# Optimization experiments

Hardware: AMD Instinct MI355X
Metric: run time of the kernel (lower is better)

## Reference

```python
import jax, jax.numpy as jnp
import numpy as np

LABELS_NUM_COUNT = [500000, 120000, 80000, 45000, 30000, 250000, 15000, 9000,
                    60000, 7000, 180000, 22000, 11000, 95000, 5000, 40000]
B, W = 2097152, 16  # batch, num_classes


def _build_penalty_matrix():
    c = np.asarray(LABELS_NUM_COUNT, dtype=np.float32)
    P = np.maximum(c[:, None], c[None, :]) / (c[:, None] + c[None, :])
    np.fill_diagonal(P, 1.0)
    return jnp.asarray(P)  # [W, W]


def setup_inputs() -> dict:
    key = jax.random.key(0)
    k1, k2 = jax.random.split(key)
    predict = jax.random.normal(k1, (B, W), dtype=jnp.float32)
    target = jax.random.normal(k2, (B, W), dtype=jnp.float32)
    return {"predict": predict, "target": target,
            "penalty_matrix": _build_penalty_matrix()}


def reference(predict, target, penalty_matrix):
    # `logpredict` in the original is actually softmax(predict).
    probs = jax.nn.softmax(predict, axis=-1)              # [B, W]
    pre = jnp.argmax(predict, axis=-1)                    # [B] predicted class
    tar = jnp.argmax(target, axis=-1)                     # [B] target class
    # scatter_ writes 1 at the predicted slot, then the loop overwrites it with
    # penalty[tar, pre] on mismatch or 0 on match -> net weight is:
    w = jnp.where(pre == tar, jnp.float32(0.0), penalty_matrix[tar, pre])  # [B]
    # sum(onehot * probs, -1) == probs at the predicted class
    p_at_pre = jnp.take_along_axis(probs, pre[:, None], axis=-1)[:, 0]     # [B]
    return jnp.mean(w * p_at_pre)
```

## Files before the change

kernel.cpp:

```cpp
#include <hip/hip_runtime.h>

#define NROWS 2097152
#define W 16

__global__ __launch_bounds__(256) void cel_weight_kernel(
    const float* __restrict__ predict,
    const float* __restrict__ target,
    const float* __restrict__ penalty,
    float* __restrict__ out)
{
    __shared__ float s_pen[W * W];
    __shared__ float s_part[4];

    const int tid = threadIdx.x;
    if (tid < W * W) s_pen[tid] = penalty[tid];
    __syncthreads();

    float acc = 0.0f;
    const int stride = gridDim.x * blockDim.x;

    for (int r = blockIdx.x * blockDim.x + tid; r < NROWS; r += stride) {
        const float4* prow = (const float4*)(predict + (size_t)r * W);
        const float4* trow = (const float4*)(target + (size_t)r * W);
        float4 p0 = prow[0], p1 = prow[1], p2 = prow[2], p3 = prow[3];
        float4 t0 = trow[0], t1 = trow[1], t2 = trow[2], t3 = trow[3];

        float pv[W] = {p0.x, p0.y, p0.z, p0.w, p1.x, p1.y, p1.z, p1.w,
                       p2.x, p2.y, p2.z, p2.w, p3.x, p3.y, p3.z, p3.w};
        float tv[W] = {t0.x, t0.y, t0.z, t0.w, t1.x, t1.y, t1.z, t1.w,
                       t2.x, t2.y, t2.z, t2.w, t3.x, t3.y, t3.z, t3.w};

        float pmax = pv[0]; int pidx = 0;
        #pragma unroll
        for (int j = 1; j < W; ++j) {
            if (pv[j] > pmax) { pmax = pv[j]; pidx = j; }
        }
        float s = 0.0f;
        #pragma unroll
        for (int j = 0; j < W; ++j) s += __expf(pv[j] - pmax);

        float tmax = tv[0]; int tidx = 0;
        #pragma unroll
        for (int j = 1; j < W; ++j) {
            if (tv[j] > tmax) { tmax = tv[j]; tidx = j; }
        }

        float wgt = (pidx == tidx) ? 0.0f : s_pen[tidx * W + pidx];
        acc += wgt / s;
    }

    #pragma unroll
    for (int off = 32; off > 0; off >>= 1)
        acc += __shfl_down(acc, off);

    const int lane = tid & 63;
    const int wid  = tid >> 6;
    if (lane == 0) s_part[wid] = acc;
    __syncthreads();

    if (tid == 0) {
        float tot = s_part[0] + s_part[1] + s_part[2] + s_part[3];
        atomicAdd(out, tot * (1.0f / (float)NROWS));
    }
}

extern "C" void kernel_launch(void* const* d_in, const int* in_sizes, int n_in,
                              void* d_out, int out_size, void* d_ws, size_t ws_size,
                              hipStream_t stream)
{
    const float* predict = (const float*)d_in[0];
    const float* target  = (const float*)d_in[1];
    const float* penalty = (const float*)d_in[2];
    float* out = (float*)d_out;

    hipMemsetAsync(out, 0, sizeof(float) * out_size, stream);

    dim3 grid(2048), block(256);
    cel_weight_kernel<<<grid, block, 0, stream>>>(predict, target, penalty, out);
}
```

Baseline: 274.4 us.

## Split each row across four lanes with shuffle-based argmax and softmax reductions

Reassigns work so four consecutive lanes each load one float4 of a row, which makes global loads fully coalesced instead of each thread reading a 64-byte row. Per-row max, argmax and exp-sum are combined across the four lanes with xor shuffles, and four independent loads are issued per iteration to raise memory-level parallelism. The cost is extra shuffle instructions, with three of every four lanes sitting idle during accumulation. The iteration count is fixed at compile time.

```diff
diff --git a/kernel.cpp b/kernel.cpp
--- a/kernel.cpp
+++ b/kernel.cpp
@@ -2,54 +2,81 @@
 
 #define NROWS 2097152
 #define W 16
+#define TPB 256
+#define BLOCKS 2048
+#define STRIDE (BLOCKS * TPB)
+#define NF4 (NROWS * 4)
+#define NITER (NF4 / STRIDE)
+#define UNROLL 4
 
-__global__ __launch_bounds__(256) void cel_weight_kernel(
+__device__ __forceinline__ void argmax_combine(float& m, int& i, float mo, int io)
+{
+    if (mo > m || (mo == m && io < i)) { m = mo; i = io; }
+}
+
+__global__ __launch_bounds__(TPB) void cel_weight_kernel(
     const float* __restrict__ predict,
     const float* __restrict__ target,
     const float* __restrict__ penalty,
     float* __restrict__ out)
 {
     __shared__ float s_pen[W * W];
-    __shared__ float s_part[4];
+    __shared__ float s_part[TPB / 64];
 
     const int tid = threadIdx.x;
-    if (tid < W * W) s_pen[tid] = penalty[tid];
+    s_pen[tid] = penalty[tid];
     __syncthreads();
 
+    const int gid   = blockIdx.x * TPB + tid;
+    const int pos   = tid & 3;
+    const int cbase = pos << 2;
+
+    const float4* __restrict__ P4 = (const float4*)predict;
+    const float4* __restrict__ T4 = (const float4*)target;
+
     float acc = 0.0f;
-    const int stride = gridDim.x * blockDim.x;
 
-    for (int r = blockIdx.x * blockDim.x + tid; r < NROWS; r += stride) {
-        const float4* prow = (const float4*)(predict + (size_t)r * W);
-        const float4* trow = (const float4*)(target + (size_t)r * W);
-        float4 p0 = prow[0], p1 = prow[1], p2 = prow[2], p3 = prow[3];
-        float4 t0 = trow[0], t1 = trow[1], t2 = trow[2], t3 = trow[3];
-
-        float pv[W] = {p0.x, p0.y, p0.z, p0.w, p1.x, p1.y, p1.z, p1.w,
-                       p2.x, p2.y, p2.z, p2.w, p3.x, p3.y, p3.z, p3.w};
-        float tv[W] = {t0.x, t0.y, t0.z, t0.w, t1.x, t1.y, t1.z, t1.w,
-                       t2.x, t2.y, t2.z, t2.w, t3.x, t3.y, t3.z, t3.w};
-
-        float pmax = pv[0]; int pidx = 0;
-        #pragma unroll
-        for (int j = 1; j < W; ++j) {
-            if (pv[j] > pmax) { pmax = pv[j]; pidx = j; }
-        }
-        float s = 0.0f;
-        #pragma unroll
-        for (int j = 0; j < W; ++j) s += __expf(pv[j] - pmax);
-
-        float tmax = tv[0]; int tidx = 0;
-        #pragma unroll
-        for (int j = 1; j < W; ++j) {
-            if (tv[j] > tmax) { tmax = tv[j]; tidx = j; }
+    for (int it = 0; it < NITER; it += UNROLL) {
+        float4 p[UNROLL], t[UNROLL];
+#pragma unroll
+        for (int u = 0; u < UNROLL; ++u) {
+            const int f = gid + (it + u) * STRIDE;
+            p[u] = P4[f];
+            t[u] = T4[f];
         }
 
-        float wgt = (pidx == tidx) ? 0.0f : s_pen[tidx * W + pidx];
-        acc += wgt / s;
+#pragma unroll
+        for (int u = 0; u < UNROLL; ++u) {
+            const float pv0 = p[u].x, pv1 = p[u].y, pv2 = p[u].z, pv3 = p[u].w;
+
+            float pm = pv0; int pi = cbase;
+            if (pv1 > pm) { pm = pv1; pi = cbase + 1; }
+            if (pv2 > pm) { pm = pv2; pi = cbase + 2; }
+            if (pv3 > pm) { pm = pv3; pi = cbase + 3; }
+            argmax_combine(pm, pi, __shfl_xor(pm, 1), __shfl_xor(pi, 1));
+            argmax_combine(pm, pi, __shfl_xor(pm, 2), __shfl_xor(pi, 2));
+
+            float e = __expf(pv0 - pm) + __expf(pv1 - pm)
+                    + __expf(pv2 - pm) + __expf(pv3 - pm);
+            e += __shfl_xor(e, 1);
+            e += __shfl_xor(e, 2);
+
+            const float tv0 = t[u].x, tv1 = t[u].y, tv2 = t[u].z, tv3 = t[u].w;
+            float tm = tv0; int ti = cbase;
+            if (tv1 > tm) { tm = tv1; ti = cbase + 1; }
+            if (tv2 > tm) { tm = tv2; ti = cbase + 2; }
+            if (tv3 > tm) { tm = tv3; ti = cbase + 3; }
+            argmax_combine(tm, ti, __shfl_xor(tm, 1), __shfl_xor(ti, 1));
+            argmax_combine(tm, ti, __shfl_xor(tm, 2), __shfl_xor(ti, 2));
+
+            if (pos == 0) {
+                const float w = (pi == ti) ? 0.0f : s_pen[ti * W + pi];
+                acc += w / e;
+            }
+        }
     }
 
-    #pragma unroll
+#pragma unroll
     for (int off = 32; off > 0; off >>= 1)
         acc += __shfl_down(acc, off);
 
@@ -75,6 +102,6 @@
 
     hipMemsetAsync(out, 0, sizeof(float) * out_size, stream);
 
-    dim3 grid(2048), block(256);
+    dim3 grid(BLOCKS), block(TPB);
     cel_weight_kernel<<<grid, block, 0, stream>>>(predict, target, penalty, out);
 }
```

Result: slower. 283.4 us (+3.3%).

## Prefetch all rows per thread up front and use tree-based argmax

Applied to the files above, without the earlier changes.

Replaces the grid-stride loop with a fixed grid of 4096 blocks, where each thread first issues loads for all its rows (two rows) into registers and only then computes. The intent is more memory-level parallelism to better saturate HBM bandwidth on a purely streaming kernel. The sequential compare-and-select argmax becomes an fmax tree plus an equality bitmask and ffs, which shortens the dependency chain and keeps first-index tie-breaking. This costs higher register usage and hard-codes the row count into the launch shape.

```diff
diff --git a/kernel.cpp b/kernel.cpp
--- a/kernel.cpp
+++ b/kernel.cpp
@@ -2,54 +2,77 @@
 
 #define NROWS 2097152
 #define W 16
+#define TPB 256
+#define BLOCKS 4096
+#define NTHREADS (BLOCKS * TPB)
+#define RPT (NROWS / NTHREADS)
 
-__global__ __launch_bounds__(256) void cel_weight_kernel(
+__device__ __forceinline__ int argmax16(const float* v, float& mout)
+{
+    float a0 = fmaxf(v[0],  v[1]),  a1 = fmaxf(v[2],  v[3]);
+    float a2 = fmaxf(v[4],  v[5]),  a3 = fmaxf(v[6],  v[7]);
+    float a4 = fmaxf(v[8],  v[9]),  a5 = fmaxf(v[10], v[11]);
+    float a6 = fmaxf(v[12], v[13]), a7 = fmaxf(v[14], v[15]);
+    float b0 = fmaxf(a0, a1), b1 = fmaxf(a2, a3);
+    float b2 = fmaxf(a4, a5), b3 = fmaxf(a6, a7);
+    float m  = fmaxf(fmaxf(b0, b1), fmaxf(b2, b3));
+    unsigned mask = 0u;
+#pragma unroll
+    for (int j = 0; j < 16; ++j) mask |= (v[j] == m) ? (1u << j) : 0u;
+    mout = m;
+    return __ffs(mask) - 1;
+}
+
+__global__ __launch_bounds__(TPB) void cel_weight_kernel(
     const float* __restrict__ predict,
     const float* __restrict__ target,
     const float* __restrict__ penalty,
     float* __restrict__ out)
 {
     __shared__ float s_pen[W * W];
-    __shared__ float s_part[4];
+    __shared__ float s_part[TPB / 64];
 
     const int tid = threadIdx.x;
-    if (tid < W * W) s_pen[tid] = penalty[tid];
+    s_pen[tid] = penalty[tid];
     __syncthreads();
 
+    const int gid = blockIdx.x * TPB + tid;
+
+    float4 pb[RPT][4], tb[RPT][4];
+#pragma unroll
+    for (int k = 0; k < RPT; ++k) {
+        const float4* prow = (const float4*)predict + (size_t)(gid + k * NTHREADS) * 4;
+        const float4* trow = (const float4*)target  + (size_t)(gid + k * NTHREADS) * 4;
+        pb[k][0] = prow[0]; pb[k][1] = prow[1]; pb[k][2] = prow[2]; pb[k][3] = prow[3];
+        tb[k][0] = trow[0]; tb[k][1] = trow[1]; tb[k][2] = trow[2]; tb[k][3] = trow[3];
+    }
+
     float acc = 0.0f;
-    const int stride = gridDim.x * blockDim.x;
 
-    for (int r = blockIdx.x * blockDim.x + tid; r < NROWS; r += stride) {
-        const float4* prow = (const float4*)(predict + (size_t)r * W);
-        const float4* trow = (const float4*)(target + (size_t)r * W);
-        float4 p0 = prow[0], p1 = prow[1], p2 = prow[2], p3 = prow[3];
-        float4 t0 = trow[0], t1 = trow[1], t2 = trow[2], t3 = trow[3];
+#pragma unroll
+    for (int k = 0; k < RPT; ++k) {
+        const float pv[W] = {pb[k][0].x, pb[k][0].y, pb[k][0].z, pb[k][0].w,
+                             pb[k][1].x, pb[k][1].y, pb[k][1].z, pb[k][1].w,
+                             pb[k][2].x, pb[k][2].y, pb[k][2].z, pb[k][2].w,
+                             pb[k][3].x, pb[k][3].y, pb[k][3].z, pb[k][3].w};
+        const float tv[W] = {tb[k][0].x, tb[k][0].y, tb[k][0].z, tb[k][0].w,
+                             tb[k][1].x, tb[k][1].y, tb[k][1].z, tb[k][1].w,
+                             tb[k][2].x, tb[k][2].y, tb[k][2].z, tb[k][2].w,
+                             tb[k][3].x, tb[k][3].y, tb[k][3].z, tb[k][3].w};
 
-        float pv[W] = {p0.x, p0.y, p0.z, p0.w, p1.x, p1.y, p1.z, p1.w,
-                       p2.x, p2.y, p2.z, p2.w, p3.x, p3.y, p3.z, p3.w};
-        float tv[W] = {t0.x, t0.y, t0.z, t0.w, t1.x, t1.y, t1.z, t1.w,
-                       t2.x, t2.y, t2.z, t2.w, t3.x, t3.y, t3.z, t3.w};
+        float pmax, tmax;
+        const int pidx = argmax16(pv, pmax);
+        const int tidx = argmax16(tv, tmax);
 
-        float pmax = pv[0]; int pidx = 0;
-        #pragma unroll
-        for (int j = 1; j < W; ++j) {
-            if (pv[j] > pmax) { pmax = pv[j]; pidx = j; }
-        }
         float s = 0.0f;
-        #pragma unroll
+#pragma unroll
         for (int j = 0; j < W; ++j) s += __expf(pv[j] - pmax);
 
-        float tmax = tv[0]; int tidx = 0;
-        #pragma unroll
-        for (int j = 1; j < W; ++j) {
-            if (tv[j] > tmax) { tmax = tv[j]; tidx = j; }
-        }
-
-        float wgt = (pidx == tidx) ? 0.0f : s_pen[tidx * W + pidx];
-        acc += wgt / s;
+        const float w = s_pen[tidx * W + pidx];
+        acc += (pidx == tidx) ? 0.0f : w / s;
     }
 
-    #pragma unroll
+#pragma unroll
     for (int off = 32; off > 0; off >>= 1)
         acc += __shfl_down(acc, off);
 
@@ -75,6 +98,6 @@
 
     hipMemsetAsync(out, 0, sizeof(float) * out_size, stream);
 
-    dim3 grid(2048), block(256);
+    dim3 grid(BLOCKS), block(TPB);
     cel_weight_kernel<<<grid, block, 0, stream>>>(predict, target, penalty, out);
 }
```

After: 279.5 us. No clear change (+1.9%).
